# Optimization experiments

Hardware: AMD Instinct MI355X
Metric: run time of the kernel (lower is better)

Reference implementation:

```python
import jax, jax.numpy as jnp
import numpy as np

N = 50000   # atoms
E = 800000  # edges (avg degree 16)
F = 128     # n_atombasis
K = 64      # n_radialbasis
NRI = 3     # residual layers in interaction
NRA = 2     # atomic residual layers


def ssp(x):
    # PhysNet shifted softplus: softplus(x) - log(2)
    return jax.nn.softplus(x) - jnp.asarray(np.log(2.0), x.dtype)


def setup_inputs() -> dict:
    key = jax.random.key(0)
    ks = jax.random.split(key, 24)
    s = 0.05  # small weight scale (orig xavier gain=1e-4; nonzero so math is non-degenerate)
    inp = {
        "features": jax.random.normal(ks[0], (N, F), jnp.float32),
        "descriptors": jax.random.normal(ks[1], (E, K), jnp.float32),
        "idx_i": jnp.sort(jax.random.randint(ks[2], (E,), 0, N)),
        "idx_j": jax.random.randint(ks[3], (E,), 0, N),
        "Wdesc": jax.random.normal(ks[4], (F, K), jnp.float32) * s,   # desc2feat, no bias
        "Wi": jax.random.normal(ks[5], (F, F), jnp.float32) * s,
        "bi": jnp.zeros((F,), jnp.float32),
        "Wj": jax.random.normal(ks[6], (F, F), jnp.float32) * s,
        "bj": jnp.zeros((F,), jnp.float32),
        "Wri1": jax.random.normal(ks[7], (NRI, F, F), jnp.float32) * s,
        "bri1": jnp.zeros((NRI, F), jnp.float32),
        "Wri2": jax.random.normal(ks[8], (NRI, F, F), jnp.float32) * s,
        "bri2": jnp.zeros((NRI, F), jnp.float32),
        "Wd": jax.random.normal(ks[9], (F, F), jnp.float32) * s,
        "bd": jnp.zeros((F,), jnp.float32),
        "u": jnp.ones((F,), jnp.float32),
        "Wra1": jax.random.normal(ks[10], (NRA, F, F), jnp.float32) * s,
        "bra1": jnp.zeros((NRA, F), jnp.float32),
        "Wra2": jax.random.normal(ks[11], (NRA, F, F), jnp.float32) * s,
        "bra2": jnp.zeros((NRA, F), jnp.float32),
    }
    return inp


def _residual(m, W1, b1, W2, b2):
    # ResidualLayer (eval mode, no dropout): m + residual(dense(act(m)))
    y = ssp(m)
    h = ssp(y @ W1.T + b1)  # dense (with activation)
    return m + h @ W2.T + b2  # residual (no activation)


def reference(features, descriptors, Wdesc, Wi, bi, Wj, bj,
              Wri1, bri1, Wri2, bri2, Wd, bd, u,
              Wra1, bra1, Wra2, bra2, idx_i, idx_j):
    x = features                               # [N, F]
    xa = ssp(x)
    g = descriptors @ Wdesc.T                  # [E, F] edge gate
    xi = ssp(xa @ Wi.T + bi)                   # [N, F]
    xj_all = ssp(xa @ Wj.T + bj)               # [N, F]
    pxj = g * xj_all[idx_j]                    # gather -> elementwise mul, [E, F]
    xj = jax.ops.segment_sum(pxj, idx_i, num_segments=x.shape[0])  # scatter-add [N, F]
    message = xi + xj
    for k in range(NRI):
        message = _residual(message, Wri1[k], bri1[k], Wri2[k], bri2[k])
    message = ssp(message)
    x = u * x + message @ Wd.T + bd
    for k in range(NRA):
        x = _residual(x, Wra1[k], bra1[k], Wra2[k], bra2[k])
    return x
```

## Files before the change

### kernel.cpp

```cpp
#include <hip/hip_runtime.h>
#include <math.h>

#define NA 50000
#define NE 800000
#define FDIM 128
#define KDIM 64
#define NRI 3
#define NRA 2
#define ETILES 10

typedef unsigned short ushort_t;
typedef unsigned int uint_t;
typedef __attribute__((ext_vector_type(8))) short short8v;
typedef __attribute__((ext_vector_type(4))) float f32x4;
typedef __attribute__((ext_vector_type(4))) unsigned short u16x4;

__device__ __forceinline__ float ssp_f(float x) {
    float e = __expf(-fabsf(x));
    return fmaxf(x, 0.0f) + __logf(1.0f + e) - 0.69314718055994530942f;
}
__device__ __forceinline__ ushort_t f2bf(float x) {
    unsigned u = __float_as_uint(x);
    u += 0x7FFFu + ((u >> 16) & 1u);
    return (ushort_t)(u >> 16);
}
__device__ __forceinline__ float bf2f(ushort_t h) {
    return __uint_as_float(((unsigned)h) << 16);
}
__device__ __forceinline__ f32x4 ssp4(f32x4 v) {
    f32x4 r;
    #pragma unroll
    for (int j = 0; j < 4; ++j) r[j] = ssp_f(v[j]);
    return r;
}
__device__ __forceinline__ u16x4 pack4(f32x4 v) {
    u16x4 p;
    #pragma unroll
    for (int j = 0; j < 4; ++j) p[j] = f2bf(v[j]);
    return p;
}

__global__ __launch_bounds__(256) void k_wconv(
    const float* __restrict__ Wdesc, const float* __restrict__ Wi,
    const float* __restrict__ Wj,    const float* __restrict__ Wri1,
    const float* __restrict__ Wri2,  const float* __restrict__ Wd,
    const float* __restrict__ Wra1,  const float* __restrict__ Wra2,
    ushort_t* __restrict__ wbf)
{
    const int seg = blockIdx.y;
    const int idx = blockIdx.x * 2048 + threadIdx.x * 8;
    const float* s; ushort_t* d; int cnt;
    const int CH = 40960;
    switch (seg) {
    case 0: cnt = 8192;  if (idx >= cnt) return; s = Wdesc + idx; d = wbf + idx; break;
    case 1: cnt = 16384; if (idx >= cnt) return; s = Wi + idx;    d = wbf + 8192 + idx; break;
    case 2: cnt = 16384; if (idx >= cnt) return; s = Wj + idx;    d = wbf + 24576 + idx; break;
    case 3: { cnt = 3*16384; if (idx >= cnt) return; int k = idx/16384, o = idx - k*16384;
              s = Wri1 + idx; d = wbf + CH + (2*k)*16384 + o; break; }
    case 4: { cnt = 3*16384; if (idx >= cnt) return; int k = idx/16384, o = idx - k*16384;
              s = Wri2 + idx; d = wbf + CH + (2*k+1)*16384 + o; break; }
    case 5: cnt = 16384; if (idx >= cnt) return; s = Wd + idx; d = wbf + CH + 6*16384 + idx; break;
    case 6: { cnt = 2*16384; if (idx >= cnt) return; int k = idx/16384, o = idx - k*16384;
              s = Wra1 + idx; d = wbf + CH + (7+2*k)*16384 + o; break; }
    default:{ cnt = 2*16384; if (idx >= cnt) return; int k = idx/16384, o = idx - k*16384;
              s = Wra2 + idx; d = wbf + CH + (8+2*k)*16384 + o; break; }
    }
    #pragma unroll
    for (int j = 0; j < 8; ++j) d[j] = f2bf(s[j]);
}

__device__ __forceinline__ void stage_w(const ushort_t* __restrict__ src,
                                        ushort_t (*wlds)[136], int t)
{
    const int r = t >> 1, c0 = (t & 1) * 64;
    const short8v* s = (const short8v*)(src + (size_t)r * FDIM + c0);
    #pragma unroll
    for (int q = 0; q < 8; ++q)
        *(short8v*)&wlds[r][c0 + q * 8] = s[q];
}

__device__ __forceinline__ void gemm_tile_T(
    const ushort_t (*actA)[136], const ushort_t (*wlds)[136],
    int w, int lrow, int kgrp, const float* __restrict__ bias, f32x4 acc[8])
{
    short8v bfr[4];
    #pragma unroll
    for (int ks = 0; ks < 4; ++ks)
        bfr[ks] = *(const short8v*)&actA[16 * w + lrow][ks * 32 + kgrp * 8];
    #pragma unroll
    for (int nf = 0; nf < 8; ++nf)
        acc[nf] = *(const f32x4*)(bias + 16 * nf + 4 * kgrp);
    #pragma unroll
    for (int nf = 0; nf < 8; ++nf)
        #pragma unroll
        for (int ks = 0; ks < 4; ++ks) {
            short8v av = *(const short8v*)&wlds[16 * nf + lrow][ks * 32 + kgrp * 8];
            acc[nf] = __builtin_amdgcn_mfma_f32_16x16x32_bf16(av, bfr[ks], acc[nf], 0, 0, 0);
        }
}

__device__ __forceinline__ void write_act_T(
    ushort_t (*actA)[136], int w, int lrow, int kgrp, const f32x4 v[8])
{
    #pragma unroll
    for (int nf = 0; nf < 8; ++nf)
        *(u16x4*)&actA[16 * w + lrow][16 * nf + 4 * kgrp] = pack4(ssp4(v[nf]));
}

__global__ __launch_bounds__(256) void k_node_pre(
    const float* __restrict__ feat, const ushort_t* __restrict__ wbf,
    const float* __restrict__ bi, const float* __restrict__ bj,
    float* __restrict__ xi_out, ushort_t* __restrict__ xja_out)
{
    __shared__ ushort_t actA[64][136];
    __shared__ ushort_t wlds[128][136];
    const int t = threadIdx.x, lane = t & 63, w = t >> 6;
    const int lrow = lane & 15, kgrp = lane >> 4;
    const int atom = blockIdx.x * 64 + 16 * w + lrow;
    const bool ok = atom < NA;

    f32x4 v[8];
    #pragma unroll
    for (int nf = 0; nf < 8; ++nf)
        v[nf] = ok ? *(const f32x4*)(feat + (size_t)atom * FDIM + 16 * nf + 4 * kgrp)
                   : (f32x4){0.f, 0.f, 0.f, 0.f};
    write_act_T(actA, w, lrow, kgrp, v);
    __syncthreads();
    stage_w(wbf + 8192, wlds, t);
    __syncthreads();
    f32x4 acc[8];
    gemm_tile_T(actA, wlds, w, lrow, kgrp, bi, acc);
    if (ok)
        #pragma unroll
        for (int nf = 0; nf < 8; ++nf)
            *(f32x4*)(xi_out + (size_t)atom * FDIM + 16 * nf + 4 * kgrp) = ssp4(acc[nf]);
    __syncthreads();
    stage_w(wbf + 24576, wlds, t);
    __syncthreads();
    gemm_tile_T(actA, wlds, w, lrow, kgrp, bj, acc);
    if (ok)
        #pragma unroll
        for (int nf = 0; nf < 8; ++nf)
            *(u16x4*)(xja_out + (size_t)atom * FDIM + 16 * nf + 4 * kgrp) = pack4(ssp4(acc[nf]));
}

__device__ __forceinline__ short8v pack8(const float* p) {
    short8v r;
    #pragma unroll
    for (int j = 0; j < 8; ++j) r[j] = (short)f2bf(p[j]);
    return r;
}

#define LOAD_DESC(T0, T1, ern)                                        \
    {                                                                 \
        const float* q_ = desc + (size_t)(ern) * KDIM + kgrp * 8;     \
        *(float4*)(T0)     = *(const float4*)q_;                      \
        *(float4*)(T0 + 4) = *(const float4*)(q_ + 4);                \
        *(float4*)(T1)     = *(const float4*)(q_ + 32);               \
        *(float4*)(T1 + 4) = *(const float4*)(q_ + 36);               \
    }

#define EDGE_TILE(T0, T1, JJCUR, JJOTH, BUF, TT)                              \
    {                                                                         \
        if (t < 64) ii[BUF][t] = idx_i[ebase + (TT) * 64 + t];                \
        short8v b0 = pack8(T0), b1 = pack8(T1);                               \
        f32x4 acc[8];                                                         \
        _Pragma("unroll")                                                     \
        for (int nf = 0; nf < 8; ++nf) acc[nf] = (f32x4){0.f,0.f,0.f,0.f};    \
        _Pragma("unroll")                                                     \
        for (int nf = 0; nf < 8; ++nf) {                                      \
            acc[nf] = __builtin_amdgcn_mfma_f32_16x16x32_bf16(a[nf][0], b0, acc[nf],0,0,0); \
            acc[nf] = __builtin_amdgcn_mfma_f32_16x16x32_bf16(a[nf][1], b1, acc[nf],0,0,0); \
        }                                                                     \
        _Pragma("unroll")                                                     \
        for (int nf = 0; nf < 8; ++nf) {                                      \
            f32x4 pr;                                                         \
            _Pragma("unroll")                                                 \
            for (int j = 0; j < 4; ++j) pr[j] = acc[nf][j] * bf2f(xv[nf][j]); \
            *(u16x4*)&pl[BUF][w * 16 + lrow][16 * nf + 4 * kgrp] = pack4(pr); \
        }                                                                     \
        if ((TT) + 2 < ETILES) {                                              \
            int ern_ = ebase + ((TT) + 2) * 64 + eoff;                        \
            JJCUR = idx_j[ern_];                                              \
            LOAD_DESC(T0, T1, ern_)                                           \
        }                                                                     \
        if ((TT) + 1 < ETILES) {                                              \
            _Pragma("unroll")                                                 \
            for (int nf = 0; nf < 8; ++nf)                                    \
                xv[nf] = *(const u16x4*)(xja + (size_t)(JJOTH) * FDIM + 16 * nf + 4 * kgrp); \
        }                                                                     \
        __syncthreads();                                                      \
        _Pragma("unroll")                                                     \
        for (int g = 0; g < 8; ++g) {                                         \
            float vv[4]; int id[4];                                           \
            _Pragma("unroll")                                                 \
            for (int qq = 0; qq < 4; ++qq) {                                  \
                vv[qq] = bf2f(pl[BUF][r0 + g * 4 + qq][f]);                   \
                id[qq] = ii[BUF][r0 + g * 4 + qq];                            \
            }                                                                 \
            _Pragma("unroll")                                                 \
            for (int qq = 0; qq < 4; ++qq) {                                  \
                if (id[qq] != scur) {                                         \
                    if (scur >= 0) unsafeAtomicAdd(&msg[(size_t)scur * FDIM + f], sacc); \
                    sacc = 0.0f; scur = id[qq];                               \
                }                                                             \
                sacc += vv[qq];                                               \
            }                                                                 \
        }                                                                     \
    }

__global__ __launch_bounds__(256) void k_edge_fused(
    const float* __restrict__ desc, const ushort_t* __restrict__ wdbf,
    const int* __restrict__ idx_i, const int* __restrict__ idx_j,
    const ushort_t* __restrict__ xja,
    float* __restrict__ msg)
{
    __shared__ ushort_t pl[2][64][136];
    __shared__ int ii[2][64];
    const int t = threadIdx.x, lane = t & 63, w = t >> 6;
    const int lrow = lane & 15, kgrp = lane >> 4;
    const int ebase = blockIdx.x * (64 * ETILES);
    const int eoff = w * 16 + lrow;

    short8v a[8][2];
    #pragma unroll
    for (int nf = 0; nf < 8; ++nf)
        #pragma unroll
        for (int ks = 0; ks < 2; ++ks)
            a[nf][ks] = *(const short8v*)(wdbf + (size_t)(16 * nf + lrow) * KDIM
                                          + ks * 32 + kgrp * 8);

    float tA0[8], tA1[8], tB0[8], tB1[8];
    int jjA = idx_j[ebase + eoff];
    LOAD_DESC(tA0, tA1, ebase + eoff)
    int jjB = idx_j[ebase + 64 + eoff];
    LOAD_DESC(tB0, tB1, ebase + 64 + eoff)
    u16x4 xv[8];
    #pragma unroll
    for (int nf = 0; nf < 8; ++nf)
        xv[nf] = *(const u16x4*)(xja + (size_t)jjA * FDIM + 16 * nf + 4 * kgrp);

    const int f = t & 127, h = t >> 7;
    const int r0 = h * 32;
    float sacc = 0.0f;
    int scur = -1;

    for (int tt = 0; tt < ETILES; tt += 2) {
        EDGE_TILE(tA0, tA1, jjA, jjB, 0, tt)
        EDGE_TILE(tB0, tB1, jjB, jjA, 1, tt + 1)
    }
    if (scur >= 0) unsafeAtomicAdd(&msg[(size_t)scur * FDIM + f], sacc);
}

__global__ __launch_bounds__(256) void k_chain(
    const float* __restrict__ msgp, const float* __restrict__ feat,
    const float* __restrict__ u, const ushort_t* __restrict__ wch,
    const float* __restrict__ bri1, const float* __restrict__ bri2,
    const float* __restrict__ bd,
    const float* __restrict__ bra1, const float* __restrict__ bra2,
    float* __restrict__ xout)
{
    __shared__ ushort_t actA[64][136];
    __shared__ ushort_t wlds[128][136];
    const int t = threadIdx.x, lane = t & 63, w = t >> 6;
    const int lrow = lane & 15, kgrp = lane >> 4;
    const int atom = blockIdx.x * 64 + 16 * w + lrow;
    const bool ok = atom < NA;

    f32x4 m[8], h[8], acc[8];
    #pragma unroll
    for (int nf = 0; nf < 8; ++nf)
        m[nf] = ok ? *(const f32x4*)(msgp + (size_t)atom * FDIM + 16 * nf + 4 * kgrp)
                   : (f32x4){0.f, 0.f, 0.f, 0.f};

    for (int k = 0; k < NRI; ++k) {
        write_act_T(actA, w, lrow, kgrp, m);
        __syncthreads();
        stage_w(wch + (size_t)(2 * k) * 16384, wlds, t);
        __syncthreads();
        gemm_tile_T(actA, wlds, w, lrow, kgrp, bri1 + k * FDIM, acc);
        #pragma unroll
        for (int nf = 0; nf < 8; ++nf) h[nf] = acc[nf];
        write_act_T(actA, w, lrow, kgrp, h);
        __syncthreads();
        stage_w(wch + (size_t)(2 * k + 1) * 16384, wlds, t);
        __syncthreads();
        gemm_tile_T(actA, wlds, w, lrow, kgrp, bri2 + k * FDIM, acc);
        #pragma unroll
        for (int nf = 0; nf < 8; ++nf) m[nf] += acc[nf];
    }

    write_act_T(actA, w, lrow, kgrp, m);
    __syncthreads();
    stage_w(wch + (size_t)6 * 16384, wlds, t);
    __syncthreads();
    gemm_tile_T(actA, wlds, w, lrow, kgrp, bd, acc);
    #pragma unroll
    for (int nf = 0; nf < 8; ++nf) {
        f32x4 fv = ok ? *(const f32x4*)(feat + (size_t)atom * FDIM + 16 * nf + 4 * kgrp)
                      : (f32x4){0.f, 0.f, 0.f, 0.f};
        f32x4 uv = *(const f32x4*)(u + 16 * nf + 4 * kgrp);
        m[nf] = uv * fv + acc[nf];
    }

    for (int k = 0; k < NRA; ++k) {
        write_act_T(actA, w, lrow, kgrp, m);
        __syncthreads();
        stage_w(wch + (size_t)(7 + 2 * k) * 16384, wlds, t);
        __syncthreads();
        gemm_tile_T(actA, wlds, w, lrow, kgrp, bra1 + k * FDIM, acc);
        #pragma unroll
        for (int nf = 0; nf < 8; ++nf) h[nf] = acc[nf];
        write_act_T(actA, w, lrow, kgrp, h);
        __syncthreads();
        stage_w(wch + (size_t)(8 + 2 * k) * 16384, wlds, t);
        __syncthreads();
        gemm_tile_T(actA, wlds, w, lrow, kgrp, bra2 + k * FDIM, acc);
        #pragma unroll
        for (int nf = 0; nf < 8; ++nf) m[nf] += acc[nf];
    }

    if (ok)
        #pragma unroll
        for (int nf = 0; nf < 8; ++nf)
            *(f32x4*)(xout + (size_t)atom * FDIM + 16 * nf + 4 * kgrp) = m[nf];
}

extern "C" void kernel_launch(void* const* d_in, const int* in_sizes, int n_in,
                              void* d_out, int out_size, void* d_ws, size_t ws_size,
                              hipStream_t stream)
{
    const float* feat  = (const float*)d_in[0];
    const float* desc  = (const float*)d_in[1];
    const int*   idx_i = (const int*)d_in[2];
    const int*   idx_j = (const int*)d_in[3];
    const float* Wdesc = (const float*)d_in[4];
    const float* Wi    = (const float*)d_in[5];
    const float* bi    = (const float*)d_in[6];
    const float* Wj    = (const float*)d_in[7];
    const float* bj    = (const float*)d_in[8];
    const float* Wri1  = (const float*)d_in[9];
    const float* bri1  = (const float*)d_in[10];
    const float* Wri2  = (const float*)d_in[11];
    const float* bri2  = (const float*)d_in[12];
    const float* Wd    = (const float*)d_in[13];
    const float* bd    = (const float*)d_in[14];
    const float* u     = (const float*)d_in[15];
    const float* Wra1  = (const float*)d_in[16];
    const float* bra1  = (const float*)d_in[17];
    const float* Wra2  = (const float*)d_in[18];
    const float* bra2  = (const float*)d_in[19];

    char* wsp = (char*)d_ws;
    float* msg = (float*)wsp;
    size_t off = (size_t)NA * FDIM * sizeof(float);
    ushort_t* xja = (ushort_t*)(wsp + off);
    off += (size_t)NA * FDIM * sizeof(ushort_t);
    ushort_t* wbf = (ushort_t*)(wsp + off);
    off += (((size_t)221184 * sizeof(ushort_t)) + 255) & ~(size_t)255;

    float* xout = (float*)d_out;
    const int nblk64 = (NA + 63) / 64;

    k_wconv<<<dim3(24, 8), 256, 0, stream>>>(Wdesc, Wi, Wj, Wri1, Wri2, Wd, Wra1, Wra2, wbf);
    k_node_pre<<<nblk64, 256, 0, stream>>>(feat, wbf, bi, bj, msg, xja);
    k_edge_fused<<<NE / (64 * ETILES), 256, 0, stream>>>(desc, wbf, idx_i, idx_j, xja, msg);
    k_chain<<<nblk64, 256, 0, stream>>>(msg, feat, u, wbf + 40960,
                                        bri1, bri2, bd, bra1, bra2, xout);
}
```

Before: 233.0 us.

## Process 128 atoms per chain block to reuse staged weights twice

The chain kernel now handles two 64-atom row groups per block, so every staged 128x128 weight tile in LDS serves twice as many rows. The grid is halved. Staging weights and the barriers around it now happen once per 128 atoms instead of once per 64. The residual and atomic layers are folded into one loop, and the hidden activation is written back in place over the input rows. The cost is double the activation LDS and more live registers per thread, which may lower occupancy.

```diff
diff --git a/kernel.cpp b/kernel.cpp
--- a/kernel.cpp
+++ b/kernel.cpp
@@ -79,14 +79,14 @@
         *(short8v*)&wlds[r][c0 + q * 8] = s[q];
 }
 
-__device__ __forceinline__ void gemm_tile_T(
+__device__ __forceinline__ void gemm_row(
     const ushort_t (*actA)[136], const ushort_t (*wlds)[136],
-    int w, int lrow, int kgrp, const float* __restrict__ bias, f32x4 acc[8])
+    int row, int lrow, int kgrp, const float* __restrict__ bias, f32x4 acc[8])
 {
     short8v bfr[4];
     #pragma unroll
     for (int ks = 0; ks < 4; ++ks)
-        bfr[ks] = *(const short8v*)&actA[16 * w + lrow][ks * 32 + kgrp * 8];
+        bfr[ks] = *(const short8v*)&actA[row][ks * 32 + kgrp * 8];
     #pragma unroll
     for (int nf = 0; nf < 8; ++nf)
         acc[nf] = *(const f32x4*)(bias + 16 * nf + 4 * kgrp);
@@ -99,12 +99,12 @@
         }
 }
 
-__device__ __forceinline__ void write_act_T(
-    ushort_t (*actA)[136], int w, int lrow, int kgrp, const f32x4 v[8])
-{
-    #pragma unroll
-    for (int nf = 0; nf < 8; ++nf)
-        *(u16x4*)&actA[16 * w + lrow][16 * nf + 4 * kgrp] = pack4(ssp4(v[nf]));
+__device__ __forceinline__ void write_act_row(
+    ushort_t (*actA)[136], int row, int kgrp, const f32x4 v[8])
+{
+    #pragma unroll
+    for (int nf = 0; nf < 8; ++nf)
+        *(u16x4*)&actA[row][16 * nf + 4 * kgrp] = pack4(ssp4(v[nf]));
 }
 
 __global__ __launch_bounds__(256) void k_node_pre(
@@ -116,7 +116,8 @@
     __shared__ ushort_t wlds[128][136];
     const int t = threadIdx.x, lane = t & 63, w = t >> 6;
     const int lrow = lane & 15, kgrp = lane >> 4;
-    const int atom = blockIdx.x * 64 + 16 * w + lrow;
+    const int row = 16 * w + lrow;
+    const int atom = blockIdx.x * 64 + row;
     const bool ok = atom < NA;
 
     f32x4 v[8];
@@ -124,12 +125,12 @@
     for (int nf = 0; nf < 8; ++nf)
         v[nf] = ok ? *(const f32x4*)(feat + (size_t)atom * FDIM + 16 * nf + 4 * kgrp)
                    : (f32x4){0.f, 0.f, 0.f, 0.f};
-    write_act_T(actA, w, lrow, kgrp, v);
+    write_act_row(actA, row, kgrp, v);
     __syncthreads();
     stage_w(wbf + 8192, wlds, t);
     __syncthreads();
     f32x4 acc[8];
-    gemm_tile_T(actA, wlds, w, lrow, kgrp, bi, acc);
+    gemm_row(actA, wlds, row, lrow, kgrp, bi, acc);
     if (ok)
         #pragma unroll
         for (int nf = 0; nf < 8; ++nf)
@@ -137,7 +138,7 @@
     __syncthreads();
     stage_w(wbf + 24576, wlds, t);
     __syncthreads();
-    gemm_tile_T(actA, wlds, w, lrow, kgrp, bj, acc);
+    gemm_row(actA, wlds, row, lrow, kgrp, bj, acc);
     if (ok)
         #pragma unroll
         for (int nf = 0; nf < 8; ++nf)
@@ -260,70 +261,83 @@
     const float* __restrict__ bra1, const float* __restrict__ bra2,
     float* __restrict__ xout)
 {
-    __shared__ ushort_t actA[64][136];
+    __shared__ ushort_t actA[128][136];
     __shared__ ushort_t wlds[128][136];
     const int t = threadIdx.x, lane = t & 63, w = t >> 6;
     const int lrow = lane & 15, kgrp = lane >> 4;
-    const int atom = blockIdx.x * 64 + 16 * w + lrow;
-    const bool ok = atom < NA;
-
-    f32x4 m[8], h[8], acc[8];
-    #pragma unroll
-    for (int nf = 0; nf < 8; ++nf)
-        m[nf] = ok ? *(const f32x4*)(msgp + (size_t)atom * FDIM + 16 * nf + 4 * kgrp)
-                   : (f32x4){0.f, 0.f, 0.f, 0.f};
-
-    for (int k = 0; k < NRI; ++k) {
-        write_act_T(actA, w, lrow, kgrp, m);
-        __syncthreads();
-        stage_w(wch + (size_t)(2 * k) * 16384, wlds, t);
-        __syncthreads();
-        gemm_tile_T(actA, wlds, w, lrow, kgrp, bri1 + k * FDIM, acc);
-        #pragma unroll
-        for (int nf = 0; nf < 8; ++nf) h[nf] = acc[nf];
-        write_act_T(actA, w, lrow, kgrp, h);
-        __syncthreads();
-        stage_w(wch + (size_t)(2 * k + 1) * 16384, wlds, t);
-        __syncthreads();
-        gemm_tile_T(actA, wlds, w, lrow, kgrp, bri2 + k * FDIM, acc);
-        #pragma unroll
-        for (int nf = 0; nf < 8; ++nf) m[nf] += acc[nf];
-    }
-
-    write_act_T(actA, w, lrow, kgrp, m);
-    __syncthreads();
-    stage_w(wch + (size_t)6 * 16384, wlds, t);
-    __syncthreads();
-    gemm_tile_T(actA, wlds, w, lrow, kgrp, bd, acc);
+    const int rowA = 16 * w + lrow, rowB = 64 + rowA;
+    const int atomA = blockIdx.x * 128 + rowA;
+    const int atomB = atomA + 64;
+    const bool okA = atomA < NA, okB = atomB < NA;
+
+    f32x4 mA[8], mB[8], acc[8];
     #pragma unroll
     for (int nf = 0; nf < 8; ++nf) {
-        f32x4 fv = ok ? *(const f32x4*)(feat + (size_t)atom * FDIM + 16 * nf + 4 * kgrp)
-                      : (f32x4){0.f, 0.f, 0.f, 0.f};
-        f32x4 uv = *(const f32x4*)(u + 16 * nf + 4 * kgrp);
-        m[nf] = uv * fv + acc[nf];
-    }
-
-    for (int k = 0; k < NRA; ++k) {
-        write_act_T(actA, w, lrow, kgrp, m);
-        __syncthreads();
-        stage_w(wch + (size_t)(7 + 2 * k) * 16384, wlds, t);
-        __syncthreads();
-        gemm_tile_T(actA, wlds, w, lrow, kgrp, bra1 + k * FDIM, acc);
-        #pragma unroll
-        for (int nf = 0; nf < 8; ++nf) h[nf] = acc[nf];
-        write_act_T(actA, w, lrow, kgrp, h);
-        __syncthreads();
-        stage_w(wch + (size_t)(8 + 2 * k) * 16384, wlds, t);
-        __syncthreads();
-        gemm_tile_T(actA, wlds, w, lrow, kgrp, bra2 + k * FDIM, acc);
-        #pragma unroll
-        for (int nf = 0; nf < 8; ++nf) m[nf] += acc[nf];
-    }
-
-    if (ok)
+        mA[nf] = okA ? *(const f32x4*)(msgp + (size_t)atomA * FDIM + 16 * nf + 4 * kgrp)
+                     : (f32x4){0.f, 0.f, 0.f, 0.f};
+        mB[nf] = okB ? *(const f32x4*)(msgp + (size_t)atomB * FDIM + 16 * nf + 4 * kgrp)
+                     : (f32x4){0.f, 0.f, 0.f, 0.f};
+    }
+
+    for (int k = 0; k < NRI + NRA; ++k) {
+        const int s1 = (k < NRI) ? 2 * k     : 7 + 2 * (k - NRI);
+        const int s2 = (k < NRI) ? 2 * k + 1 : 8 + 2 * (k - NRI);
+        const float* b1 = (k < NRI) ? bri1 + k * FDIM : bra1 + (k - NRI) * FDIM;
+        const float* b2 = (k < NRI) ? bri2 + k * FDIM : bra2 + (k - NRI) * FDIM;
+
+        write_act_row(actA, rowA, kgrp, mA);
+        write_act_row(actA, rowB, kgrp, mB);
+        __syncthreads();
+        stage_w(wch + (size_t)s1 * 16384, wlds, t);
+        __syncthreads();
+        gemm_row(actA, wlds, rowA, lrow, kgrp, b1, acc);
+        write_act_row(actA, rowA, kgrp, acc);
+        gemm_row(actA, wlds, rowB, lrow, kgrp, b1, acc);
+        write_act_row(actA, rowB, kgrp, acc);
+        __syncthreads();
+        stage_w(wch + (size_t)s2 * 16384, wlds, t);
+        __syncthreads();
+        gemm_row(actA, wlds, rowA, lrow, kgrp, b2, acc);
+        #pragma unroll
+        for (int nf = 0; nf < 8; ++nf) mA[nf] += acc[nf];
+        gemm_row(actA, wlds, rowB, lrow, kgrp, b2, acc);
+        #pragma unroll
+        for (int nf = 0; nf < 8; ++nf) mB[nf] += acc[nf];
+
+        if (k == NRI - 1) {
+            write_act_row(actA, rowA, kgrp, mA);
+            write_act_row(actA, rowB, kgrp, mB);
+            __syncthreads();
+            stage_w(wch + (size_t)6 * 16384, wlds, t);
+            __syncthreads();
+            gemm_row(actA, wlds, rowA, lrow, kgrp, bd, acc);
+            #pragma unroll
+            for (int nf = 0; nf < 8; ++nf) {
+                f32x4 fv = okA ? *(const f32x4*)(feat + (size_t)atomA * FDIM + 16 * nf + 4 * kgrp)
+                               : (f32x4){0.f, 0.f, 0.f, 0.f};
+                f32x4 uv = *(const f32x4*)(u + 16 * nf + 4 * kgrp);
+                mA[nf] = uv * fv + acc[nf];
+            }
+            gemm_row(actA, wlds, rowB, lrow, kgrp, bd, acc);
+            #pragma unroll
+            for (int nf = 0; nf < 8; ++nf) {
+                f32x4 fv = okB ? *(const f32x4*)(feat + (size_t)atomB * FDIM + 16 * nf + 4 * kgrp)
+                               : (f32x4){0.f, 0.f, 0.f, 0.f};
+                f32x4 uv = *(const f32x4*)(u + 16 * nf + 4 * kgrp);
+                mB[nf] = uv * fv + acc[nf];
+            }
+        }
+        __syncthreads();
+    }
+
+    if (okA)
         #pragma unroll
         for (int nf = 0; nf < 8; ++nf)
-            *(f32x4*)(xout + (size_t)atom * FDIM + 16 * nf + 4 * kgrp) = m[nf];
+            *(f32x4*)(xout + (size_t)atomA * FDIM + 16 * nf + 4 * kgrp) = mA[nf];
+    if (okB)
+        #pragma unroll
+        for (int nf = 0; nf < 8; ++nf)
+            *(f32x4*)(xout + (size_t)atomB * FDIM + 16 * nf + 4 * kgrp) = mB[nf];
 }
 
 extern "C" void kernel_launch(void* const* d_in, const int* in_sizes, int n_in,
@@ -361,10 +375,11 @@
 
     float* xout = (float*)d_out;
     const int nblk64 = (NA + 63) / 64;
+    const int nblk128 = (NA + 127) / 128;
 
     k_wconv<<<dim3(24, 8), 256, 0, stream>>>(Wdesc, Wi, Wj, Wri1, Wri2, Wd, Wra1, Wra2, wbf);
     k_node_pre<<<nblk64, 256, 0, stream>>>(feat, wbf, bi, bj, msg, xja);
     k_edge_fused<<<NE / (64 * ETILES), 256, 0, stream>>>(desc, wbf, idx_i, idx_j, xja, msg);
-    k_chain<<<nblk64, 256, 0, stream>>>(msg, feat, u, wbf + 40960,
-                                        bri1, bri2, bd, bra1, bra2, xout);
-}
+    k_chain<<<nblk128, 256, 0, stream>>>(msg, feat, u, wbf + 40960,
+                                         bri1, bri2, bd, bra1, bra2, xout);
+}
```

Result: slower. 261.4 us (+12.2%).
